# Kernel optimization log

Hardware: AMD Instinct MI355X
Metric: run time of the kernel (lower is better)

Reference implementation:

```python
import jax, jax.numpy as jnp
import numpy as np

EMBED_DIM = 768
N_HEADS = 12
HEAD_DIM = EMBED_DIM // N_HEADS


def setup_inputs() -> dict:
    key = jax.random.key(0)
    ks = jax.random.split(key, 5)
    s = 1.0 / np.sqrt(EMBED_DIM)
    x = jax.random.normal(ks[0], (8, 1024, EMBED_DIM), dtype=jnp.float32)
    w_qkv = jax.random.normal(ks[1], (EMBED_DIM, 3 * EMBED_DIM), dtype=jnp.float32) * s
    b_qkv = jnp.zeros((3 * EMBED_DIM,), dtype=jnp.float32)
    w_proj = jax.random.normal(ks[2], (EMBED_DIM, EMBED_DIM), dtype=jnp.float32) * s
    b_proj = jnp.zeros((EMBED_DIM,), dtype=jnp.float32)
    return {"x": x, "w_qkv": w_qkv, "b_qkv": b_qkv, "w_proj": w_proj, "b_proj": b_proj}


def reference(x, w_qkv, b_qkv, w_proj, b_proj):
    B, S, D = x.shape
    H, Hd = N_HEADS, HEAD_DIM
    qkv = x @ w_qkv + b_qkv                      # [B,S,3D]
    qkv = qkv.reshape(B, S, 3, H, Hd).transpose(2, 0, 3, 1, 4)  # [3,B,H,S,Hd]
    q, k, v = qkv[0], qkv[1], qkv[2]
    scale = Hd ** -0.5
    attn = jnp.einsum('bhqd,bhkd->bhqk', q, k) * scale  # [B,H,S,S]
    attn = jax.nn.softmax(attn, axis=-1)
    out = jnp.einsum('bhqk,bhkd->bhqd', attn, v)        # [B,H,S,Hd]
    out = out.transpose(0, 2, 1, 3).reshape(B, S, D)
    return out @ w_proj + b_proj
```

## Files before the change

kernel.cpp:

```cpp
#include <hip/hip_runtime.h>
#include <stdint.h>

typedef unsigned short ushort_t;
typedef __bf16 bf16x8 __attribute__((ext_vector_type(8)));
typedef float floatx4 __attribute__((ext_vector_type(4)));

#define B_   8
#define S_   1024
#define D_   768
#define H_   12
#define M_   (B_ * S_)
#define N3_  (3 * D_)
#define QK_  1536
#define QSCALE 0.18033688f

static __device__ __forceinline__ void gl_lds16(const void* g, void* l) {
  __builtin_amdgcn_global_load_lds((const __attribute__((address_space(1))) void*)g,
                                   (__attribute__((address_space(3))) void*)l,
                                   16, 0, 0);
}

static __device__ __forceinline__ ushort_t f2bf(float f) {
  __bf16 h = (__bf16)f;
  return __builtin_bit_cast(unsigned short, h);
}

static __device__ __forceinline__ void store_out(ushort_t* p, float v) { *p = f2bf(v); }
static __device__ __forceinline__ void store_out(float* p, float v) { *p = v; }

static __device__ __forceinline__ void transpose_tile(const float* __restrict__ W,
                                                      ushort_t* __restrict__ Wt,
                                                      int K, int N, int bx, int by,
                                                      int t) {
  __shared__ float tile[32][33];
  const int n0 = bx * 32, k0 = by * 32;
  const int tx = t & 31, ty = t >> 5;
#pragma unroll
  for (int i = 0; i < 4; ++i)
    tile[ty + i * 8][tx] = W[(size_t)(k0 + ty + i * 8) * N + n0 + tx];
  __syncthreads();
#pragma unroll
  for (int i = 0; i < 4; ++i)
    Wt[(size_t)(n0 + ty + i * 8) * K + k0 + tx] = f2bf(tile[tx][ty + i * 8]);
}

__global__ __launch_bounds__(256) void prep_kernel(const float* __restrict__ x,
                                                   ushort_t* __restrict__ xb,
                                                   const float* __restrict__ w_qkv,
                                                   ushort_t* __restrict__ wqkvt,
                                                   const float* __restrict__ w_proj,
                                                   ushort_t* __restrict__ wprojt) {
  const int gb = blockIdx.x, t = threadIdx.x;
  if (gb < 6144) {
    const int i = (gb * 256 + t) * 4;
    const float4 v = *(const float4*)(x + i);
    ushort4 o4;
    o4.x = f2bf(v.x); o4.y = f2bf(v.y); o4.z = f2bf(v.z); o4.w = f2bf(v.w);
    *(ushort4*)(xb + i) = o4;
  } else if (gb < 6144 + 1728) {
    const int lb = gb - 6144;
    transpose_tile(w_qkv, wqkvt, D_, N3_, lb % 72, lb / 72, t);
  } else {
    const int lb = gb - 6144 - 1728;
    transpose_tile(w_proj, wprojt, D_, D_, lb % 24, lb / 24, t);
  }
}

template <typename OutT, bool SPLITV>
__global__ __launch_bounds__(256) void gemm_bt_bias(const ushort_t* __restrict__ A,
                                                    const ushort_t* __restrict__ Bt,
                                                    const float* __restrict__ bias,
                                                    OutT* __restrict__ C, int CN,
                                                    ushort_t* __restrict__ vt) {
  __shared__ __align__(16) ushort_t As[128 * 32];
  __shared__ __align__(16) ushort_t Bs[128 * 32];
  const int t = threadIdx.x;
  const int wave = t >> 6, lane = t & 63;
  const int quad = lane >> 4, l15 = lane & 15;
  const int wm = wave >> 1, wn = wave & 1;
  const int m0 = blockIdx.y * 128, n0 = blockIdx.x * 128;

  const int scol  = ((lane & 3) ^ ((lane >> 3) & 3)) * 8;
  const int slotq = (quad ^ ((l15 >> 1) & 3)) * 8;

  floatx4 acc[4][4];
#pragma unroll
  for (int i = 0; i < 4; ++i)
#pragma unroll
    for (int j = 0; j < 4; ++j) acc[i][j] = (floatx4)0.0f;

  for (int k0 = 0; k0 < 768; k0 += 32) {
    if (k0) __syncthreads();
#pragma unroll
    for (int c = 0; c < 2; ++c) {
      const int i0 = c * 256 + wave * 64;
      const int i = i0 + lane;
      const int row = i >> 2;
      gl_lds16(A + (size_t)(m0 + row) * 768 + k0 + scol, As + i0 * 8);
      gl_lds16(Bt + (size_t)(n0 + row) * 768 + k0 + scol, Bs + i0 * 8);
    }
    __syncthreads();

    bf16x8 af[4], bfr[4];
#pragma unroll
    for (int mi = 0; mi < 4; ++mi)
      af[mi] = *(const bf16x8*)(As + (wm * 64 + mi * 16 + l15) * 32 + slotq);
#pragma unroll
    for (int ni = 0; ni < 4; ++ni)
      bfr[ni] = *(const bf16x8*)(Bs + (wn * 64 + ni * 16 + l15) * 32 + slotq);
#pragma unroll
    for (int mi = 0; mi < 4; ++mi)
#pragma unroll
      for (int ni = 0; ni < 4; ++ni)
        acc[mi][ni] = __builtin_amdgcn_mfma_f32_16x16x32_bf16(af[mi], bfr[ni], acc[mi][ni], 0, 0, 0);
  }

#pragma unroll
  for (int ni = 0; ni < 4; ++ni) {
    const int colb = n0 + wn * 64 + ni * 16;
    const int col = colb + l15;
    const float bb = bias[col];
    if (SPLITV && colb >= 1536) {
      const int hh = (colb - 1536) >> 6;
      const int d  = ((colb - 1536) & 63) + l15;
      const int bh = (m0 >> 10) * H_ + hh;
      ushort_t* vrow = vt + ((size_t)bh * 64 + d) * 1024 +
                       (m0 & 1023) + wm * 64 + quad * 4;
#pragma unroll
      for (int mi = 0; mi < 4; ++mi) {
        ushort4 pk;
        pk.x = f2bf(acc[mi][ni][0] + bb);
        pk.y = f2bf(acc[mi][ni][1] + bb);
        pk.z = f2bf(acc[mi][ni][2] + bb);
        pk.w = f2bf(acc[mi][ni][3] + bb);
        *(ushort4*)(vrow + mi * 16) = pk;
      }
    } else {
      const float sc = (SPLITV && colb < 768) ? QSCALE : 1.0f;
#pragma unroll
      for (int mi = 0; mi < 4; ++mi) {
#pragma unroll
        for (int r = 0; r < 4; ++r) {
          const int row = m0 + wm * 64 + mi * 16 + quad * 4 + r;
          store_out(&C[(size_t)row * CN + col], (acc[mi][ni][r] + bb) * sc);
        }
      }
    }
  }
}

__global__ __launch_bounds__(256, 4) void attn_kernel(const ushort_t* __restrict__ qk,
                                                      const ushort_t* __restrict__ vt,
                                                      ushort_t* __restrict__ o) {
  __shared__ __align__(16) ushort_t Qs[64 * 64];
  __shared__ __align__(16) ushort_t Ks[64 * 64];
  __shared__ __align__(16) ushort_t Vts[64 * 64];
  __shared__ __align__(16) ushort_t Ps[64 * 72];

  const int t = threadIdx.x;
  const int wave = t >> 6, lane = t & 63;
  const int quad = lane >> 4, l15 = lane & 15;

  const int g = blockIdx.x;
  const int xcd = g & 7, gi = g >> 3;
  const int bh = xcd * 12 + (gi >> 4);
  const int q0 = (gi & 15) * 64;
  const int h = bh % H_;
  const int bS = (bh / H_) * S_;
  const ushort_t* vbase = vt + (size_t)bh * 64 * 1024;

#pragma unroll
  for (int c = 0; c < 2; ++c) {
    const int i0 = c * 256 + wave * 64;
    const int i = i0 + lane;
    const int row = i >> 3, sg = (i & 7) ^ (row & 7);
    gl_lds16(qk + (size_t)(bS + q0 + row) * QK_ + h * 64 + sg * 8, Qs + i0 * 8);
    gl_lds16(qk + (size_t)(bS + row) * QK_ + 768 + h * 64 + sg * 8, Ks + i0 * 8);
    gl_lds16(vbase + (size_t)row * 1024 + sg * 8, Vts + i0 * 8);
  }
  __syncthreads();

  bf16x8 qf[2];
#pragma unroll
  for (int kb = 0; kb < 2; ++kb)
    qf[kb] = *(const bf16x8*)(Qs + (wave * 16 + l15) * 64 +
                              (((kb * 4 + quad) ^ (l15 & 7)) * 8));

  floatx4 oa[4];
#pragma unroll
  for (int d = 0; d < 4; ++d) oa[d] = (floatx4)0.0f;
  float lsum[4] = {0.f, 0.f, 0.f, 0.f};

  for (int kv0 = 0; kv0 < S_; kv0 += 64) {
    if (kv0) {
      __syncthreads();
#pragma unroll
      for (int c = 0; c < 2; ++c) {
        const int i0 = c * 256 + wave * 64;
        const int i = i0 + lane;
        const int row = i >> 3, sg = (i & 7) ^ (row & 7);
        gl_lds16(qk + (size_t)(bS + kv0 + row) * QK_ + 768 + h * 64 + sg * 8,
                 Ks + i0 * 8);
        gl_lds16(vbase + (size_t)row * 1024 + kv0 + sg * 8, Vts + i0 * 8);
      }
      __syncthreads();
    }

    floatx4 sa[4];
#pragma unroll
    for (int ni = 0; ni < 4; ++ni) sa[ni] = (floatx4)0.0f;
#pragma unroll
    for (int ni = 0; ni < 4; ++ni)
#pragma unroll
      for (int kb = 0; kb < 2; ++kb) {
        const bf16x8 kf = *(const bf16x8*)(Ks + (ni * 16 + l15) * 64 +
                                           (((kb * 4 + quad) ^ (l15 & 7)) * 8));
        sa[ni] = __builtin_amdgcn_mfma_f32_16x16x32_bf16(qf[kb], kf, sa[ni], 0, 0, 0);
      }

#pragma unroll
    for (int r = 0; r < 4; ++r) {
      float psum = 0.0f;
#pragma unroll
      for (int ni = 0; ni < 4; ++ni) {
        const float p = exp2f(sa[ni][r]);
        psum += p;
        Ps[(wave * 16 + quad * 4 + r) * 72 + ni * 16 + l15] = f2bf(p);
      }
      lsum[r] += psum;
    }

#pragma unroll
    for (int kb = 0; kb < 2; ++kb) {
      const bf16x8 pf = *(const bf16x8*)(Ps + (wave * 16 + l15) * 72 +
                                         kb * 32 + quad * 8);
#pragma unroll
      for (int dt = 0; dt < 4; ++dt) {
        const bf16x8 vf = *(const bf16x8*)(Vts + (dt * 16 + l15) * 64 +
                                           (((kb * 4 + quad) ^ (l15 & 7)) * 8));
        oa[dt] = __builtin_amdgcn_mfma_f32_16x16x32_bf16(pf, vf, oa[dt], 0, 0, 0);
      }
    }
  }

#pragma unroll
  for (int r = 0; r < 4; ++r) {
#pragma unroll
    for (int off = 8; off >= 1; off >>= 1)
      lsum[r] += __shfl_xor(lsum[r], off, 64);
  }

#pragma unroll
  for (int dt = 0; dt < 4; ++dt)
#pragma unroll
    for (int r = 0; r < 4; ++r) {
      const int q = q0 + wave * 16 + quad * 4 + r;
      o[(size_t)(bS + q) * D_ + h * 64 + dt * 16 + l15] =
          f2bf(oa[dt][r] / lsum[r]);
    }
}

extern "C" void kernel_launch(void* const* d_in, const int* in_sizes, int n_in,
                              void* d_out, int out_size, void* d_ws, size_t ws_size,
                              hipStream_t stream) {
  const float* x      = (const float*)d_in[0];
  const float* w_qkv  = (const float*)d_in[1];
  const float* b_qkv  = (const float*)d_in[2];
  const float* w_proj = (const float*)d_in[3];
  const float* b_proj = (const float*)d_in[4];
  float* out = (float*)d_out;

  ushort_t* xb = (ushort_t*)d_out;

  ushort_t* vtb    = (ushort_t*)d_ws;
  ushort_t* wqkvt  = vtb + (size_t)96 * 64 * 1024;
  ushort_t* wprojt = wqkvt + (size_t)N3_ * D_;
  ushort_t* qkb    = wprojt + (size_t)D_ * D_;
  ushort_t* attnb  = qkb + (size_t)M_ * QK_;

  prep_kernel<<<6144 + 1728 + 576, 256, 0, stream>>>(x, xb, w_qkv, wqkvt,
                                                     w_proj, wprojt);
  gemm_bt_bias<ushort_t, true><<<dim3(N3_ / 128, M_ / 128), 256, 0, stream>>>(
      xb, wqkvt, b_qkv, qkb, QK_, vtb);
  attn_kernel<<<dim3(1536), 256, 0, stream>>>(qkb, vtb, attnb);
  gemm_bt_bias<float, false><<<dim3(D_ / 128, M_ / 128), 256, 0, stream>>>(
      attnb, wprojt, b_proj, out, D_, nullptr);
}
```

Baseline: 209.1 us.

## Rewrite attention with 32x32 MFMA, in-register P via permlane swap, 128-row Q tiles

Restructures the attention kernel to use 32x32x16 bf16 MFMA, computing S transposed (K as A operand) so P stays in registers. P is converted with v_cvt_pk_bf16 and rearranged with v_permlane32_swap into the A-operand layout, removing the LDS round trip for P. Each block now handles 128 query rows (32 per wave), halving the grid and the number of K/V loads per query. The cost is higher register pressure, with launch bounds relaxed to 3 blocks per SM, and fewer blocks overall.

```diff
diff --git a/kernel.cpp b/kernel.cpp
--- a/kernel.cpp
+++ b/kernel.cpp
@@ -4,6 +4,8 @@
 typedef unsigned short ushort_t;
 typedef __bf16 bf16x8 __attribute__((ext_vector_type(8)));
 typedef float floatx4 __attribute__((ext_vector_type(4)));
+typedef float floatx16 __attribute__((ext_vector_type(16)));
+typedef unsigned int uintx4 __attribute__((ext_vector_type(4)));
 
 #define B_   8
 #define S_   1024
@@ -27,6 +29,15 @@
 
 static __device__ __forceinline__ void store_out(ushort_t* p, float v) { *p = f2bf(v); }
 static __device__ __forceinline__ void store_out(float* p, float v) { *p = v; }
+
+static __device__ __forceinline__ unsigned cvt_pk_bf16(float lo, float hi) {
+  unsigned d;
+  asm("v_cvt_pk_bf16_f32 %0, %1, %2" : "=v"(d) : "v"(lo), "v"(hi));
+  return d;
+}
+static __device__ __forceinline__ void plane32_swap(unsigned& a, unsigned& b) {
+  asm volatile("v_permlane32_swap_b32 %0, %1" : "+v"(a), "+v"(b));
+}
 
 static __device__ __forceinline__ void transpose_tile(const float* __restrict__ W,
                                                       ushort_t* __restrict__ Wt,
@@ -149,47 +160,53 @@
   }
 }
 
-__global__ __launch_bounds__(256, 4) void attn_kernel(const ushort_t* __restrict__ qk,
+__global__ __launch_bounds__(256, 3) void attn_kernel(const ushort_t* __restrict__ qk,
                                                       const ushort_t* __restrict__ vt,
                                                       ushort_t* __restrict__ o) {
-  __shared__ __align__(16) ushort_t Qs[64 * 64];
+  __shared__ __align__(16) ushort_t Qs[128 * 64];
   __shared__ __align__(16) ushort_t Ks[64 * 64];
   __shared__ __align__(16) ushort_t Vts[64 * 64];
-  __shared__ __align__(16) ushort_t Ps[64 * 72];
+  __shared__ float Ls[128];
 
   const int t = threadIdx.x;
   const int wave = t >> 6, lane = t & 63;
-  const int quad = lane >> 4, l15 = lane & 15;
+  const int l31 = lane & 31, hi = lane >> 5, l7 = lane & 7;
 
   const int g = blockIdx.x;
   const int xcd = g & 7, gi = g >> 3;
-  const int bh = xcd * 12 + (gi >> 4);
-  const int q0 = (gi & 15) * 64;
+  const int bh = xcd * 12 + (gi >> 3);
+  const int q0 = (gi & 7) * 128;
   const int h = bh % H_;
   const int bS = (bh / H_) * S_;
   const ushort_t* vbase = vt + (size_t)bh * 64 * 1024;
 
+#pragma unroll
+  for (int c = 0; c < 4; ++c) {
+    const int i0 = c * 256 + wave * 64;
+    const int i = i0 + lane;
+    const int row = i >> 3, sg = (i & 7) ^ (row & 7);
+    gl_lds16(qk + (size_t)(bS + q0 + row) * QK_ + h * 64 + sg * 8, Qs + i0 * 8);
+  }
 #pragma unroll
   for (int c = 0; c < 2; ++c) {
     const int i0 = c * 256 + wave * 64;
     const int i = i0 + lane;
     const int row = i >> 3, sg = (i & 7) ^ (row & 7);
-    gl_lds16(qk + (size_t)(bS + q0 + row) * QK_ + h * 64 + sg * 8, Qs + i0 * 8);
     gl_lds16(qk + (size_t)(bS + row) * QK_ + 768 + h * 64 + sg * 8, Ks + i0 * 8);
     gl_lds16(vbase + (size_t)row * 1024 + sg * 8, Vts + i0 * 8);
   }
   __syncthreads();
 
-  bf16x8 qf[2];
-#pragma unroll
-  for (int kb = 0; kb < 2; ++kb)
-    qf[kb] = *(const bf16x8*)(Qs + (wave * 16 + l15) * 64 +
-                              (((kb * 4 + quad) ^ (l15 & 7)) * 8));
-
-  floatx4 oa[4];
-#pragma unroll
-  for (int d = 0; d < 4; ++d) oa[d] = (floatx4)0.0f;
-  float lsum[4] = {0.f, 0.f, 0.f, 0.f};
+  bf16x8 qf[4];
+#pragma unroll
+  for (int ks = 0; ks < 4; ++ks)
+    qf[ks] = *(const bf16x8*)(Qs + (wave * 32 + l31) * 64 +
+                              (((ks * 2 + hi) ^ l7) * 8));
+
+  floatx16 oa[2];
+  oa[0] = (floatx16)0.0f;
+  oa[1] = (floatx16)0.0f;
+  float lsum = 0.0f;
 
   for (int kv0 = 0; kv0 < S_; kv0 += 64) {
     if (kv0) {
@@ -206,58 +223,64 @@
       __syncthreads();
     }
 
-    floatx4 sa[4];
-#pragma unroll
-    for (int ni = 0; ni < 4; ++ni) sa[ni] = (floatx4)0.0f;
-#pragma unroll
-    for (int ni = 0; ni < 4; ++ni)
-#pragma unroll
-      for (int kb = 0; kb < 2; ++kb) {
-        const bf16x8 kf = *(const bf16x8*)(Ks + (ni * 16 + l15) * 64 +
-                                           (((kb * 4 + quad) ^ (l15 & 7)) * 8));
-        sa[ni] = __builtin_amdgcn_mfma_f32_16x16x32_bf16(qf[kb], kf, sa[ni], 0, 0, 0);
-      }
-
-#pragma unroll
-    for (int r = 0; r < 4; ++r) {
-      float psum = 0.0f;
-#pragma unroll
-      for (int ni = 0; ni < 4; ++ni) {
-        const float p = exp2f(sa[ni][r]);
-        psum += p;
-        Ps[(wave * 16 + quad * 4 + r) * 72 + ni * 16 + l15] = f2bf(p);
-      }
-      lsum[r] += psum;
-    }
-
-#pragma unroll
-    for (int kb = 0; kb < 2; ++kb) {
-      const bf16x8 pf = *(const bf16x8*)(Ps + (wave * 16 + l15) * 72 +
-                                         kb * 32 + quad * 8);
-#pragma unroll
-      for (int dt = 0; dt < 4; ++dt) {
-        const bf16x8 vf = *(const bf16x8*)(Vts + (dt * 16 + l15) * 64 +
-                                           (((kb * 4 + quad) ^ (l15 & 7)) * 8));
-        oa[dt] = __builtin_amdgcn_mfma_f32_16x16x32_bf16(pf, vf, oa[dt], 0, 0, 0);
-      }
-    }
-  }
-
-#pragma unroll
-  for (int r = 0; r < 4; ++r) {
-#pragma unroll
-    for (int off = 8; off >= 1; off >>= 1)
-      lsum[r] += __shfl_xor(lsum[r], off, 64);
-  }
-
-#pragma unroll
-  for (int dt = 0; dt < 4; ++dt)
-#pragma unroll
-    for (int r = 0; r < 4; ++r) {
-      const int q = q0 + wave * 16 + quad * 4 + r;
-      o[(size_t)(bS + q) * D_ + h * 64 + dt * 16 + l15] =
-          f2bf(oa[dt][r] / lsum[r]);
-    }
+    floatx16 sw0 = (floatx16)0.0f, sw1 = (floatx16)0.0f;
+#pragma unroll
+    for (int ks = 0; ks < 4; ++ks) {
+      const bf16x8 kf0 = *(const bf16x8*)(Ks + (l31) * 64 + (((ks * 2 + hi) ^ l7) * 8));
+      const bf16x8 kf1 = *(const bf16x8*)(Ks + (32 + l31) * 64 + (((ks * 2 + hi) ^ l7) * 8));
+      sw0 = __builtin_amdgcn_mfma_f32_32x32x16_bf16(kf0, qf[ks], sw0, 0, 0, 0);
+      sw1 = __builtin_amdgcn_mfma_f32_32x32x16_bf16(kf1, qf[ks], sw1, 0, 0, 0);
+    }
+
+    uintx4 pw[4];
+#pragma unroll
+    for (int tkv = 0; tkv < 2; ++tkv) {
+      float p[16];
+      float ps = 0.0f;
+#pragma unroll
+      for (int r = 0; r < 16; ++r) {
+        p[r] = exp2f(tkv ? sw1[r] : sw0[r]);
+        ps += p[r];
+      }
+      lsum += ps;
+#pragma unroll
+      for (int sub = 0; sub < 2; ++sub) {
+        const int b = sub * 8;
+        unsigned a0 = cvt_pk_bf16(p[b + 0], p[b + 1]);
+        unsigned b0 = cvt_pk_bf16(p[b + 4], p[b + 5]);
+        plane32_swap(a0, b0);
+        unsigned a1 = cvt_pk_bf16(p[b + 2], p[b + 3]);
+        unsigned b1 = cvt_pk_bf16(p[b + 6], p[b + 7]);
+        plane32_swap(a1, b1);
+        uintx4 w;
+        w[0] = a0; w[1] = a1; w[2] = b0; w[3] = b1;
+        pw[tkv * 2 + sub] = w;
+      }
+    }
+
+#pragma unroll
+    for (int dt = 0; dt < 2; ++dt)
+#pragma unroll
+      for (int ks4 = 0; ks4 < 4; ++ks4) {
+        const bf16x8 vf = *(const bf16x8*)(Vts + (dt * 32 + l31) * 64 +
+                                           (((ks4 * 2 + hi) ^ l7) * 8));
+        const bf16x8 paf = __builtin_bit_cast(bf16x8, pw[ks4]);
+        oa[dt] = __builtin_amdgcn_mfma_f32_32x32x16_bf16(paf, vf, oa[dt], 0, 0, 0);
+      }
+  }
+
+  lsum += __shfl_xor(lsum, 32, 64);
+  if (lane < 32) Ls[wave * 32 + lane] = lsum;
+
+#pragma unroll
+  for (int reg = 0; reg < 16; ++reg) {
+    const int qrow = (reg & 3) + 8 * (reg >> 2) + 4 * hi;
+    const float inv = 1.0f / Ls[wave * 32 + qrow];
+    const int q = q0 + wave * 32 + qrow;
+#pragma unroll
+    for (int dt = 0; dt < 2; ++dt)
+      o[(size_t)(bS + q) * D_ + h * 64 + dt * 32 + l31] = f2bf(oa[dt][reg] * inv);
+  }
 }
 
 extern "C" void kernel_launch(void* const* d_in, const int* in_sizes, int n_in,
@@ -282,7 +305,7 @@
                                                      w_proj, wprojt);
   gemm_bt_bias<ushort_t, true><<<dim3(N3_ / 128, M_ / 128), 256, 0, stream>>>(
       xb, wqkvt, b_qkv, qkb, QK_, vtb);
-  attn_kernel<<<dim3(1536), 256, 0, stream>>>(qkb, vtb, attnb);
+  attn_kernel<<<dim3(768), 256, 0, stream>>>(qkb, vtb, attnb);
   gemm_bt_bias<float, false><<<dim3(D_ / 128, M_ / 128), 256, 0, stream>>>(
       attnb, wprojt, b_proj, out, D_, nullptr);
 }
```

Result: faster. 199.1 us (-4.8%).
